# Optimization experiments

Measured on AMD Instinct MI355X. Metric: run time of the kernel, lower is better.

Reference implementation:

```python
import jax, jax.numpy as jnp
import numpy as np

B = 4          # per_gpu_batch_size
P = 16         # n_contexts
N = B * P      # fused passage dim = 64
L = 512        # seq_len
H = 768        # hidden_size
S = 16         # sentence spans per passage


def setup_inputs() -> dict:
    key = jax.random.key(0)
    k1, k2, k3 = jax.random.split(key, 3)
    hidden_states = jax.random.normal(k1, (N, L, H), jnp.float32)
    # nn.Linear weight [out, in]; original init std=1.0 saturates tanh, use 0.02 scale for sane numerics
    dense_w = jax.random.normal(k2, (H, H), jnp.float32) * 0.02
    dense_b = jnp.zeros((H,), jnp.float32)
    attention_mask = jnp.ones((N, L), jnp.int32)
    # strictly increasing boundaries -> S non-empty, ragged, contiguous spans per passage
    r = jnp.sort(jax.random.randint(k3, (N, S + 1), 0, L - S), axis=-1) + jnp.arange(S + 1, dtype=jnp.int32)
    spans = jnp.stack([r[:, :-1], r[:, 1:]], axis=-1).astype(jnp.int32)  # [N, S, 2]
    return dict(hidden_states=hidden_states, dense_w=dense_w, dense_b=dense_b,
                attention_mask=attention_mask, spans=spans)


def reference(hidden_states, dense_w, dense_b, attention_mask, spans):
    # sentence_spans branch: token_tensor = hidden_states (all tokens)
    # pooled_output = activation(dense(token_tensor)); cls_norm_type == 'none' -> no norm
    pooled = jnp.tanh(jnp.einsum('nlh,oh->nlo', hidden_states, dense_w) + dense_b)  # [N, L, H]
    pooled_output_passages = pooled[:, 0]  # [N, H]
    # ragged per-span mean pooling, vectorized as a masked segment reduce
    pos = jnp.arange(L, dtype=jnp.int32)                         # [L]
    start = spans[..., 0][..., None]                             # [N, S, 1]
    end = spans[..., 1][..., None]                               # [N, S, 1]
    m = ((pos >= start) & (pos < end)).astype(pooled.dtype)      # [N, S, L]
    sums = jnp.einsum('nsl,nlh->nsh', m, pooled)                 # [N, S, H]
    counts = (spans[..., 1] - spans[..., 0]).astype(pooled.dtype)[..., None]  # [N, S, 1]
    sentence_embeddings = (sums / counts).reshape(N * S, H)      # [N*S, H]
    # all S spans valid per passage -> mask of zeros (0 = valid in original code)
    sentence_mask = jnp.zeros((N, S), jnp.float32)
    return pooled_output_passages, sentence_embeddings, sentence_mask
```

## Files before the change

### kernel.cpp

```cpp
#include <hip/hip_runtime.h>
#include <hip/hip_bf16.h>

#define NPASS 64
#define LSEQ  512
#define HDIM  768
#define NSPAN 16
#define MTOT  (NPASS*LSEQ)
#define OFF_SENT (NPASS*HDIM)
#define W_ELEMS (HDIM*HDIM)

#define BM 128
#define BN 128
#define BK 32
#define NK (HDIM/BK)

typedef __bf16 bf16x8 __attribute__((ext_vector_type(8)));
typedef __bf16 bf16x4 __attribute__((ext_vector_type(4)));
typedef float  f32x4  __attribute__((ext_vector_type(4)));

__device__ inline unsigned short f2bf(float f) {
  __hip_bfloat16 h = __float2bfloat16(f);
  unsigned short u; __builtin_memcpy(&u, &h, 2); return u;
}

__device__ inline float fast_tanh(float x) {
  const float ax = fabsf(x);
  const float t  = __expf(-2.0f * ax);
  const float r  = (1.0f - t) * __builtin_amdgcn_rcpf(1.0f + t);
  return copysignf(r, x);
}

__device__ inline bf16x8 cvt8(f32x4 lo, f32x4 hi) {
  union { bf16x4 h[2]; bf16x8 v; } u;
  u.h[0] = __builtin_convertvector(lo, bf16x4);
  u.h[1] = __builtin_convertvector(hi, bf16x4);
  return u.v;
}

__global__ __launch_bounds__(256) void convert_w_kernel(
    const float* __restrict__ W, unsigned short* __restrict__ Wb)
{
  const int i = (blockIdx.x * 256 + threadIdx.x) * 8;
  const float4 a = *(const float4*)(W + i);
  const float4 b = *(const float4*)(W + i + 4);
  union { unsigned short us[8]; uint4 v; } o;
  o.us[0]=f2bf(a.x); o.us[1]=f2bf(a.y); o.us[2]=f2bf(a.z); o.us[3]=f2bf(a.w);
  o.us[4]=f2bf(b.x); o.us[5]=f2bf(b.y); o.us[6]=f2bf(b.z); o.us[7]=f2bf(b.w);
  *(uint4*)(Wb + i) = o.v;
}

__global__ __launch_bounds__(256) void gemm_fused_kernel(
    const float* __restrict__ A,
    const unsigned short* __restrict__ Wb,
    const float* __restrict__ bias,
    const int* __restrict__ spans,
    float* __restrict__ out)
{
  __shared__ __align__(16) float          As[2][BM*BK];
  __shared__ __align__(16) unsigned short Bs[2][BN*BK];
  __shared__ int   sp_st[NSPAN], sp_en[NSPAN];
  __shared__ float inv_s[NSPAN];
  __shared__ short sid_l[BM];
  __shared__ float bias_s[BN];

  const int tid  = threadIdx.x;
  const int wave = tid >> 6;
  const int lane = tid & 63;
  const int quad = lane >> 4;
  const int lr   = lane & 15;
  const int wm   = wave >> 1;
  const int wn   = wave & 1;
  const int tile_m = blockIdx.x * BM;
  const int tile_n = blockIdx.y * BN;
  const int npass  = tile_m >> 9;
  const int l0     = tile_m & 511;

  auto stage = [&](int k, int buf) {
    const int k0 = k * BK;
    #pragma unroll
    for (int j = 0; j < 6; ++j) {
      const int seg = j * 4 + wave;
      if (seg < 16) {
        const int row = seg * 8 + (lane >> 3);
        const int gs  = (lane & 7) ^ ((lane >> 3) & 7);
        const float* g = A + (size_t)(tile_m + row) * HDIM + (k0 + gs * 4);
        __builtin_amdgcn_global_load_lds(
            (const __attribute__((address_space(1))) void*)g,
            (__attribute__((address_space(3))) void*)(As[buf] + seg * 256),
            16, 0, 0);
      } else {
        const int s2  = seg - 16;
        const int row = s2 * 16 + (lane >> 2);
        const int gs  = (lane & 3) ^ ((lane >> 3) & 3);
        const unsigned short* g =
            Wb + (size_t)(tile_n + row) * HDIM + (k0 + gs * 8);
        __builtin_amdgcn_global_load_lds(
            (const __attribute__((address_space(1))) void*)g,
            (__attribute__((address_space(3))) void*)(Bs[buf] + s2 * 512),
            16, 0, 0);
      }
    }
  };

  stage(0, 0);
  if (tid < NSPAN) {
    const int st = spans[(npass * NSPAN + tid) * 2 + 0];
    const int en = spans[(npass * NSPAN + tid) * 2 + 1];
    sp_st[tid] = st; sp_en[tid] = en; inv_s[tid] = 1.0f / (float)(en - st);
  }
  if (tid >= 128 && tid < 128 + BN) bias_s[tid - 128] = bias[tile_n + tid - 128];
  __syncthreads();
  if (tid < BM) {
    const int l = l0 + tid;
    short s = -1;
    #pragma unroll
    for (int i = 0; i < NSPAN; ++i)
      if (l >= sp_st[i] && l < sp_en[i]) s = (short)i;
    sid_l[tid] = s;
  }

  f32x4 acc[4][4];
  #pragma unroll
  for (int i = 0; i < 4; ++i)
    #pragma unroll
    for (int j = 0; j < 4; ++j)
      acc[i][j] = (f32x4){0.f, 0.f, 0.f, 0.f};

  for (int k = 0; k < NK; ++k) {
    const int cur = k & 1;
    if (k + 1 < NK) stage(k + 1, cur ^ 1);

    bf16x8 af[4], bfr[4];
    #pragma unroll
    for (int mt = 0; mt < 4; ++mt) {
      const int r  = wm * 64 + mt * 16 + lr;
      const int sw = r & 7;
      const float* base = As[cur] + r * BK;
      const f32x4 lo = *(const f32x4*)(base + (((quad * 2    ) ^ sw) * 4));
      const f32x4 hi = *(const f32x4*)(base + (((quad * 2 + 1) ^ sw) * 4));
      af[mt] = cvt8(lo, hi);
    }
    #pragma unroll
    for (int nt = 0; nt < 4; ++nt) {
      const int r = wn * 64 + nt * 16 + lr;
      const int g = quad ^ ((r >> 1) & 3);
      bfr[nt] = *(const bf16x8*)(Bs[cur] + (r * BK + g * 8));
    }

    #pragma unroll
    for (int mt = 0; mt < 4; ++mt)
      #pragma unroll
      for (int nt = 0; nt < 4; ++nt)
        acc[mt][nt] = __builtin_amdgcn_mfma_f32_16x16x32_bf16(
            af[mt], bfr[nt], acc[mt][nt], 0, 0, 0);

    __syncthreads();
  }

  #pragma unroll
  for (int nt = 0; nt < 4; ++nt) {
    const int lcolo = wn * 64 + nt * 16 + lr;
    const int col   = tile_n + lcolo;
    const float bv  = bias_s[lcolo];
    float* sent_col = out + OFF_SENT + (size_t)(npass * NSPAN) * HDIM + col;
    #pragma unroll
    for (int mt = 0; mt < 4; ++mt) {
      const int rowbase = wm * 64 + mt * 16 + quad * 4;
      int prev = -1; float run = 0.f;
      #pragma unroll
      for (int r = 0; r < 4; ++r) {
        const int lrw = rowbase + r;
        const float v = fast_tanh(acc[mt][nt][r] + bv);
        if (l0 == 0 && lrw == 0) out[(size_t)npass * HDIM + col] = v;
        const int s = sid_l[lrw];
        if (s != prev) {
          if (prev >= 0) unsafeAtomicAdd(sent_col + (size_t)prev * HDIM, run * inv_s[prev]);
          prev = s; run = 0.f;
        }
        run += v;
      }
      if (prev >= 0) unsafeAtomicAdd(sent_col + (size_t)prev * HDIM, run * inv_s[prev]);
    }
  }
}

extern "C" void kernel_launch(void* const* d_in, const int* in_sizes, int n_in,
                              void* d_out, int out_size, void* d_ws, size_t ws_size,
                              hipStream_t stream) {
  const float* hs  = (const float*)d_in[0];
  const float* w   = (const float*)d_in[1];
  const float* bsc = (const float*)d_in[2];
  const int* spans = (const int*)d_in[4];
  float* out = (float*)d_out;

  unsigned short* Wb = (unsigned short*)d_ws;

  hipMemsetAsync(d_out, 0, (size_t)out_size * sizeof(float), stream);

  convert_w_kernel<<<dim3(W_ELEMS / 8 / 256), dim3(256), 0, stream>>>(w, Wb);

  dim3 grid(MTOT / BM, HDIM / BN);
  gemm_fused_kernel<<<grid, dim3(256), 0, stream>>>(hs, Wb, bsc, spans, out);
}
```

Before: 269.7 us.

## Use full-width N tiles so each A row block is read once

Restructures the GEMM so each 512-thread block computes a 64-row strip across all 768 output columns. Each fp32 activation row is therefore loaded from HBM only once, where before it was reloaded for six column tiles. The whole bf16 weight slice for a K step is staged in LDS, and MFMA priority is raised with setprio. In exchange the weight-tile LDS traffic per block grows, per-thread register use rises (24 accumulators), and launch bounds request two blocks per CU. The grid shrinks to 512 blocks.

```diff
diff --git a/kernel.cpp b/kernel.cpp
--- a/kernel.cpp
+++ b/kernel.cpp
@@ -7,12 +7,16 @@
 #define NSPAN 16
 #define MTOT  (NPASS*LSEQ)
 #define OFF_SENT (NPASS*HDIM)
+#define OFF_MASK (OFF_SENT + NPASS*NSPAN*HDIM)
 #define W_ELEMS (HDIM*HDIM)
 
-#define BM 128
-#define BN 128
-#define BK 32
-#define NK (HDIM/BK)
+#define BM   64
+#define BK   32
+#define NK   (HDIM/BK)
+#define NBLK (MTOT/BM)
+#define THREADS 512
+#define NMT  2
+#define NTN  12
 
 typedef __bf16 bf16x8 __attribute__((ext_vector_type(8)));
 typedef __bf16 bf16x4 __attribute__((ext_vector_type(4)));
@@ -49,7 +53,7 @@
   *(uint4*)(Wb + i) = o.v;
 }
 
-__global__ __launch_bounds__(256) void gemm_fused_kernel(
+__global__ __launch_bounds__(THREADS, 2) void gemm_fused_kernel(
     const float* __restrict__ A,
     const unsigned short* __restrict__ Wb,
     const float* __restrict__ bias,
@@ -57,122 +61,120 @@
     float* __restrict__ out)
 {
   __shared__ __align__(16) float          As[2][BM*BK];
-  __shared__ __align__(16) unsigned short Bs[2][BN*BK];
-  __shared__ int   sp_st[NSPAN], sp_en[NSPAN];
+  __shared__ __align__(16) unsigned short Ws[2][HDIM*BK];
   __shared__ float inv_s[NSPAN];
+  __shared__ float bias_s[HDIM];
   __shared__ short sid_l[BM];
-  __shared__ float bias_s[BN];
 
   const int tid  = threadIdx.x;
+  const int b    = blockIdx.x;
+  const int p    = b >> 3;
+  const int l0   = (b & 7) << 6;
+  const int row0 = b * BM;
+
   const int wave = tid >> 6;
   const int lane = tid & 63;
   const int quad = lane >> 4;
   const int lr   = lane & 15;
-  const int wm   = wave >> 1;
-  const int wn   = wave & 1;
-  const int tile_m = blockIdx.x * BM;
-  const int tile_n = blockIdx.y * BN;
-  const int npass  = tile_m >> 9;
-  const int l0     = tile_m & 511;
+  const int mr   = wave >> 2;
+  const int nw   = wave & 3;
 
   auto stage = [&](int k, int buf) {
     const int k0 = k * BK;
+    {
+      const int row = wave * 8 + (lane >> 3);
+      const int g   = (lane & 7) ^ ((lane >> 3) & 7);
+      const float* src = A + (size_t)(row0 + row) * HDIM + (k0 + g * 4);
+      __builtin_amdgcn_global_load_lds(
+          (const __attribute__((address_space(1))) void*)src,
+          (__attribute__((address_space(3))) void*)(As[buf] + wave * 256),
+          16, 0, 0);
+    }
     #pragma unroll
     for (int j = 0; j < 6; ++j) {
-      const int seg = j * 4 + wave;
-      if (seg < 16) {
-        const int row = seg * 8 + (lane >> 3);
-        const int gs  = (lane & 7) ^ ((lane >> 3) & 7);
-        const float* g = A + (size_t)(tile_m + row) * HDIM + (k0 + gs * 4);
-        __builtin_amdgcn_global_load_lds(
-            (const __attribute__((address_space(1))) void*)g,
-            (__attribute__((address_space(3))) void*)(As[buf] + seg * 256),
-            16, 0, 0);
-      } else {
-        const int s2  = seg - 16;
-        const int row = s2 * 16 + (lane >> 2);
-        const int gs  = (lane & 3) ^ ((lane >> 3) & 3);
-        const unsigned short* g =
-            Wb + (size_t)(tile_n + row) * HDIM + (k0 + gs * 8);
-        __builtin_amdgcn_global_load_lds(
-            (const __attribute__((address_space(1))) void*)g,
-            (__attribute__((address_space(3))) void*)(Bs[buf] + s2 * 512),
-            16, 0, 0);
-      }
+      const int s2  = wave * 6 + j;
+      const int row = s2 * 16 + (lane >> 2);
+      const int g   = (lane & 3) ^ ((lane >> 2) & 3);
+      const unsigned short* src = Wb + (size_t)row * HDIM + (k0 + g * 8);
+      __builtin_amdgcn_global_load_lds(
+          (const __attribute__((address_space(1))) void*)src,
+          (__attribute__((address_space(3))) void*)(Ws[buf] + s2 * 512),
+          16, 0, 0);
     }
   };
 
   stage(0, 0);
-  if (tid < NSPAN) {
-    const int st = spans[(npass * NSPAN + tid) * 2 + 0];
-    const int en = spans[(npass * NSPAN + tid) * 2 + 1];
-    sp_st[tid] = st; sp_en[tid] = en; inv_s[tid] = 1.0f / (float)(en - st);
-  }
-  if (tid >= 128 && tid < 128 + BN) bias_s[tid - 128] = bias[tile_n + tid - 128];
-  __syncthreads();
+  if (tid < NSPAN)
+    inv_s[tid] = 1.0f / (float)(spans[(p * NSPAN + tid) * 2 + 1] -
+                                spans[(p * NSPAN + tid) * 2 + 0]);
   if (tid < BM) {
     const int l = l0 + tid;
     short s = -1;
     #pragma unroll
-    for (int i = 0; i < NSPAN; ++i)
-      if (l >= sp_st[i] && l < sp_en[i]) s = (short)i;
+    for (int i = 0; i < NSPAN; ++i) {
+      const int st = spans[(p * NSPAN + i) * 2 + 0];
+      const int en = spans[(p * NSPAN + i) * 2 + 1];
+      if (l >= st && l < en) s = (short)i;
+    }
     sid_l[tid] = s;
   }
-
-  f32x4 acc[4][4];
+  for (int i = tid; i < HDIM; i += THREADS) bias_s[i] = bias[i];
+  __syncthreads();
+
+  f32x4 acc[NMT][NTN];
   #pragma unroll
-  for (int i = 0; i < 4; ++i)
-    #pragma unroll
-    for (int j = 0; j < 4; ++j)
-      acc[i][j] = (f32x4){0.f, 0.f, 0.f, 0.f};
+  for (int mt = 0; mt < NMT; ++mt)
+    #pragma unroll
+    for (int nt = 0; nt < NTN; ++nt)
+      acc[mt][nt] = (f32x4){0.f, 0.f, 0.f, 0.f};
 
   for (int k = 0; k < NK; ++k) {
     const int cur = k & 1;
     if (k + 1 < NK) stage(k + 1, cur ^ 1);
 
-    bf16x8 af[4], bfr[4];
-    #pragma unroll
-    for (int mt = 0; mt < 4; ++mt) {
-      const int r  = wm * 64 + mt * 16 + lr;
-      const int sw = r & 7;
-      const float* base = As[cur] + r * BK;
-      const f32x4 lo = *(const f32x4*)(base + (((quad * 2    ) ^ sw) * 4));
-      const f32x4 hi = *(const f32x4*)(base + (((quad * 2 + 1) ^ sw) * 4));
-      af[mt] = cvt8(lo, hi);
-    }
-    #pragma unroll
-    for (int nt = 0; nt < 4; ++nt) {
-      const int r = wn * 64 + nt * 16 + lr;
-      const int g = quad ^ ((r >> 1) & 3);
-      bfr[nt] = *(const bf16x8*)(Bs[cur] + (r * BK + g * 8));
-    }
-
-    #pragma unroll
-    for (int mt = 0; mt < 4; ++mt)
+    bf16x8 abf[NMT];
+    #pragma unroll
+    for (int mt = 0; mt < NMT; ++mt) {
+      const int row = mr * 32 + mt * 16 + lr;
+      const float* base = As[cur] + row * BK;
+      const f32x4 lo = *(const f32x4*)(base + (((quad * 2    ) ^ (lr & 7)) * 4));
+      const f32x4 hi = *(const f32x4*)(base + (((quad * 2 + 1) ^ (lr & 7)) * 4));
+      abf[mt] = cvt8(lo, hi);
+    }
+    bf16x8 wf[NTN];
+    #pragma unroll
+    for (int nt = 0; nt < NTN; ++nt) {
+      const int row = nw * 192 + nt * 16 + lr;
+      wf[nt] = *(const bf16x8*)(Ws[cur] + row * BK + (quad ^ (lr & 3)) * 8);
+    }
+
+    __builtin_amdgcn_s_setprio(1);
+    #pragma unroll
+    for (int mt = 0; mt < NMT; ++mt)
       #pragma unroll
-      for (int nt = 0; nt < 4; ++nt)
+      for (int nt = 0; nt < NTN; ++nt)
         acc[mt][nt] = __builtin_amdgcn_mfma_f32_16x16x32_bf16(
-            af[mt], bfr[nt], acc[mt][nt], 0, 0, 0);
+            abf[mt], wf[nt], acc[mt][nt], 0, 0, 0);
+    __builtin_amdgcn_s_setprio(0);
 
     __syncthreads();
   }
 
   #pragma unroll
-  for (int nt = 0; nt < 4; ++nt) {
-    const int lcolo = wn * 64 + nt * 16 + lr;
-    const int col   = tile_n + lcolo;
-    const float bv  = bias_s[lcolo];
-    float* sent_col = out + OFF_SENT + (size_t)(npass * NSPAN) * HDIM + col;
-    #pragma unroll
-    for (int mt = 0; mt < 4; ++mt) {
-      const int rowbase = wm * 64 + mt * 16 + quad * 4;
+  for (int nt = 0; nt < NTN; ++nt) {
+    const int col = nw * 192 + nt * 16 + lr;
+    const float bv = bias_s[col];
+    float* sent_col = out + OFF_SENT + (size_t)(p * NSPAN) * HDIM + col;
+    #pragma unroll
+    for (int mt = 0; mt < NMT; ++mt) {
+      const int rowbase = mr * 32 + mt * 16 + quad * 4;
       int prev = -1; float run = 0.f;
       #pragma unroll
       for (int r = 0; r < 4; ++r) {
-        const int lrw = rowbase + r;
+        const int row = rowbase + r;
         const float v = fast_tanh(acc[mt][nt][r] + bv);
-        if (l0 == 0 && lrw == 0) out[(size_t)npass * HDIM + col] = v;
-        const int s = sid_l[lrw];
+        if (l0 == 0 && row == 0) out[(size_t)p * HDIM + col] = v;
+        const int s = sid_l[row];
         if (s != prev) {
           if (prev >= 0) unsafeAtomicAdd(sent_col + (size_t)prev * HDIM, run * inv_s[prev]);
           prev = s; run = 0.f;
@@ -199,6 +201,6 @@
 
   convert_w_kernel<<<dim3(W_ELEMS / 8 / 256), dim3(256), 0, stream>>>(w, Wb);
 
-  dim3 grid(MTOT / BM, HDIM / BN);
-  gemm_fused_kernel<<<grid, dim3(256), 0, stream>>>(hs, Wb, bsc, spans, out);
-}
+  gemm_fused_kernel<<<dim3(NBLK), dim3(THREADS), 0, stream>>>(
+      hs, Wb, bsc, spans, out);
+}
```

After: 281.1 us. 4.2% more time.
